# Kernel tuning notes

Measured on AMD Instinct MI355X. Metric: run time of the kernel, lower is better.

## Reference

```python
import jax, jax.numpy as jnp
import numpy as np

H, NH, HD = 1024, 16, 64
B, T, S = 2, 1024, 3
NOISE, STEP, TEMP, NSTEPS = 0.1, 0.01, 1.0, 5
LN_EPS = 1e-5


def setup_inputs() -> dict:
    key = jax.random.key(0)
    ks = jax.random.split(key, 9)
    return {
        "queries": jax.random.normal(ks[0], (B, NH, T, HD), jnp.float32),
        "keys": jax.random.normal(ks[1], (B, NH, T, HD), jnp.float32),
        "values": jax.random.normal(ks[2], (B, NH, T, HD), jnp.float32),
        "hidden_states": jax.random.normal(ks[3], (B, T, H), jnp.float32),
        "W1": jax.random.normal(ks[4], (H, H), jnp.float32) * 0.02,
        "b1": jnp.zeros((H,), jnp.float32),
        "ln_g": jnp.ones((H,), jnp.float32),
        "ln_b": jnp.zeros((H,), jnp.float32),
        "W2": jax.random.normal(ks[5], (H, H), jnp.float32) * 0.02,
        "b2": jnp.zeros((H,), jnp.float32),
        "hyp_noise": jax.random.normal(ks[6], (S, B, NH, T, HD), jnp.float32),
        "ref_noise": jax.random.normal(ks[7], (S, NSTEPS - 1, B, NH, T, HD), jnp.float32),
    }


def _attention_energy(q, k, v):
    # q: [S,B,H,T,D]; k,v: [B,H,T,D] -> energy [S,B]
    scores = jnp.einsum('sbhtd,bhud->sbhtu', q, k) / jnp.sqrt(jnp.float32(q.shape[-1]))
    attn = jax.nn.softmax(scores, axis=-1)
    out = jnp.einsum('sbhtu,bhud->sbhtd', attn, v)
    out_mag = jnp.linalg.norm(out, axis=-1).mean(axis=(2, 3))          # [S,B]
    entropy = -(attn * jnp.log(attn + 1e-8)).sum(axis=-1).mean(axis=(2, 3))
    align = (q * k[None]).sum(axis=-1).mean(axis=(2, 3))
    return out_mag - 0.1 * entropy - 0.05 * align


def reference(queries, keys, values, hidden_states, W1, b1, ln_g, ln_b, W2, b2,
              hyp_noise, ref_noise):
    # query_predictor: Linear -> LayerNorm -> ReLU -> Linear
    x = hidden_states @ W1.T + b1
    mu = x.mean(axis=-1, keepdims=True)
    var = ((x - mu) ** 2).mean(axis=-1, keepdims=True)
    x = (x - mu) / jnp.sqrt(var + LN_EPS) * ln_g + ln_b
    x = jax.nn.relu(x)
    ctx = x @ W2.T + b2                                   # [B,T,H]
    ctx = ctx.reshape(B, T, NH, HD).transpose(0, 2, 1, 3) # [B,NH,T,HD]

    # exploration hypotheses, refined jointly over the sample axis
    q = queries[None] + hyp_noise * NOISE                 # [S,B,NH,T,HD]
    for step in range(NSTEPS):
        q = q - STEP * (q - ctx[None])                    # PCN prediction-error update
        if step < NSTEPS - 1:
            q = q + ref_noise[:, step] * 0.01

    energies = _attention_energy(q, keys, values)         # [S,B]
    probs = jax.nn.softmax(-energies / TEMP, axis=0)      # [S,B]
    selected = jnp.einsum('sb,sbhtd->bhtd', probs, q)     # softmax-weighted mix
    return selected, keys, values
```

## Files before the change

kernel.cpp:

```cpp
#include <hip/hip_runtime.h>
#include <hip/hip_bf16.h>
#include <math.h>

#define NB 2
#define NHH 16
#define TT 1024
#define HDD 64
#define NSS 3
#define HH 1024
#define MMR 2048

typedef float f4 __attribute__((ext_vector_type(4)));
typedef short bf16x8 __attribute__((ext_vector_type(8)));
typedef unsigned short u16;
typedef u16 u16x4 __attribute__((ext_vector_type(4)));

__device__ inline u16 f2bf(float f) {
    union { float f; unsigned u; } v; v.f = f;
    unsigned r = (v.u + 0x7FFFu + ((v.u >> 16) & 1u)) >> 16;
    return (u16)r;
}
__device__ inline float bf2f(u16 u) {
    union { unsigned u; float f; } v; v.u = ((unsigned)u) << 16;
    return v.f;
}

__device__ inline float red16sum(float v) {
    v += __shfl_xor(v, 1);
    v += __shfl_xor(v, 2);
    v += __shfl_xor(v, 4);
    v += __shfl_xor(v, 8);
    return v;
}
__device__ inline float red64sum(float v) {
    v += __shfl_xor(v, 1);
    v += __shfl_xor(v, 2);
    v += __shfl_xor(v, 4);
    v += __shfl_xor(v, 8);
    v += __shfl_xor(v, 16);
    v += __shfl_xor(v, 32);
    return v;
}

__global__ __launch_bounds__(256) void k_cvt4(const float* __restrict__ s0, u16* __restrict__ d0,
                                              const float* __restrict__ s1, u16* __restrict__ d1,
                                              const float* __restrict__ s2, u16* __restrict__ d2,
                                              const float* __restrict__ s3, u16* __restrict__ d3,
                                              float* __restrict__ outk) {
    int b = blockIdx.x;
    if (b >= 4096) {
        int i = (b - 4096) * 256 + threadIdx.x;
        f4 v = ((const f4*)s3)[i];
        ((f4*)outk)[i] = v;
        u16x4 o;
        o[0] = f2bf(v[0] * 0.125f); o[1] = f2bf(v[1] * 0.125f);
        o[2] = f2bf(v[2] * 0.125f); o[3] = f2bf(v[3] * 0.125f);
        ((u16x4*)d3)[i] = o;
        return;
    }
    const float* s; u16* d; int base;
    if (b < 2048)      { s = s0; d = d0; base = 0; }
    else if (b < 3072) { s = s1; d = d1; base = 2048; }
    else               { s = s2; d = d2; base = 3072; }
    int i = (b - base) * 256 + threadIdx.x;
    f4 v = ((const f4*)s)[i];
    u16x4 o;
    o[0] = f2bf(v[0]); o[1] = f2bf(v[1]); o[2] = f2bf(v[2]); o[3] = f2bf(v[3]);
    ((u16x4*)d)[i] = o;
}

__global__ __launch_bounds__(256) void k_vtrans(const float* __restrict__ V,
                                                u16* __restrict__ Vt,
                                                float* __restrict__ outv) {
    __shared__ float tile[64][65];
    int bh = blockIdx.y, t0 = blockIdx.x * 64;
    int r = threadIdx.x >> 2, c0 = (threadIdx.x & 3) * 16;
    const float* vp = V + ((size_t)bh * TT + t0) * HDD;
#pragma unroll
    for (int j = 0; j < 16; j += 4) {
        f4 v = *(const f4*)(vp + r * HDD + c0 + j);
        tile[r][c0 + j + 0] = v[0]; tile[r][c0 + j + 1] = v[1];
        tile[r][c0 + j + 2] = v[2]; tile[r][c0 + j + 3] = v[3];
        *(f4*)(outv + ((size_t)bh * TT + t0 + r) * HDD + c0 + j) = v;
    }
    __syncthreads();
    int d = threadIdx.x >> 2, x0 = (threadIdx.x & 3) * 16;
    u16* op = Vt + ((size_t)bh * HDD + d) * TT + t0 + x0;
#pragma unroll
    for (int j = 0; j < 16; j += 4) {
        u16x4 o;
        o[0] = f2bf(tile[x0 + j + 0][d]); o[1] = f2bf(tile[x0 + j + 1][d]);
        o[2] = f2bf(tile[x0 + j + 2][d]); o[3] = f2bf(tile[x0 + j + 3][d]);
        *(u16x4*)(op + j) = o;
    }
}

template <int EPI>
__global__ __launch_bounds__(256) void k_gemm_bt(const u16* __restrict__ A,
                                                 const u16* __restrict__ Bm,
                                                 const float* __restrict__ bias,
                                                 const float* __restrict__ que,
                                                 float* __restrict__ out) {
    const int K = 1024, N = 1024;
    int w = threadIdx.x >> 6, l = threadIdx.x & 63, lr = l & 15, lg = l >> 4;
    int m0 = blockIdx.y * 64 + w * 16;
    int n0 = blockIdx.x * 64;
    const u16* ap = A + (size_t)(m0 + lr) * K + lg * 8;
    const u16* bp = Bm + (size_t)(n0 + lr) * K + lg * 8;
    f4 z4 = {0.f, 0.f, 0.f, 0.f};
    f4 acc[4] = {z4, z4, z4, z4};
#pragma unroll 2
    for (int kk = 0; kk < K; kk += 32) {
        bf16x8 a  = *(const bf16x8*)(ap + kk);
        bf16x8 b0 = *(const bf16x8*)(bp + kk);
        bf16x8 b1 = *(const bf16x8*)(bp + 16 * K + kk);
        bf16x8 b2 = *(const bf16x8*)(bp + 32 * K + kk);
        bf16x8 b3 = *(const bf16x8*)(bp + 48 * K + kk);
        acc[0] = __builtin_amdgcn_mfma_f32_16x16x32_bf16(a, b0, acc[0], 0, 0, 0);
        acc[1] = __builtin_amdgcn_mfma_f32_16x16x32_bf16(a, b1, acc[1], 0, 0, 0);
        acc[2] = __builtin_amdgcn_mfma_f32_16x16x32_bf16(a, b2, acc[2], 0, 0, 0);
        acc[3] = __builtin_amdgcn_mfma_f32_16x16x32_bf16(a, b3, acc[3], 0, 0, 0);
    }
    const float A5 = 0.9509900499f, CC = 1.0f - A5;
#pragma unroll
    for (int cf = 0; cf < 4; ++cf) {
        int col = n0 + cf * 16 + lr;
        float bs = bias[col];
#pragma unroll
        for (int r = 0; r < 4; ++r) {
            int row = m0 + lg * 4 + r;
            float v = acc[cf][r] + bs;
            if (EPI == 0) {
                out[(size_t)row * N + col] = v;
            } else {
                int b = row >> 10, t = row & 1023, nh = col >> 6, hd = col & 63;
                size_t oidx = (((size_t)(b * NHH + nh)) * TT + t) * HDD + hd;
                out[oidx] = A5 * que[oidx] + CC * v;
            }
        }
    }
}

__global__ __launch_bounds__(256) void k_lnrelu(const float* __restrict__ X,
                                                const float* __restrict__ g,
                                                const float* __restrict__ bta,
                                                u16* __restrict__ xr) {
    int row = blockIdx.x;
    f4 v = ((const f4*)(X + (size_t)row * HH))[threadIdx.x];
    float s = v[0] + v[1] + v[2] + v[3];
    float s2 = v[0] * v[0] + v[1] * v[1] + v[2] * v[2] + v[3] * v[3];
    s = red64sum(s);
    s2 = red64sum(s2);
    __shared__ float red[8];
    int w = threadIdx.x >> 6, l = threadIdx.x & 63;
    if (l == 0) { red[w] = s; red[w + 4] = s2; }
    __syncthreads();
    float S1 = red[0] + red[1] + red[2] + red[3];
    float S2 = red[4] + red[5] + red[6] + red[7];
    float mu = S1 * (1.0f / 1024.0f);
    float var = S2 * (1.0f / 1024.0f) - mu * mu;
    float rstd = rsqrtf(var + 1e-5f);
    f4 gv = ((const f4*)g)[threadIdx.x];
    f4 bv = ((const f4*)bta)[threadIdx.x];
    u16x4 o;
#pragma unroll
    for (int j = 0; j < 4; ++j) {
        float y = (v[j] - mu) * rstd * gv[j] + bv[j];
        y = fmaxf(y, 0.f);
        o[j] = f2bf(y);
    }
    ((u16x4*)(xr + (size_t)row * HH))[threadIdx.x] = o;
}

__global__ __launch_bounds__(256, 3) void k_attn(const float* __restrict__ basep_,
                                                 const float* __restrict__ hyp,
                                                 const float* __restrict__ rn,
                                                 const u16* __restrict__ Kb,
                                                 const u16* __restrict__ Vt,
                                                 u16* __restrict__ qq,
                                                 float* __restrict__ part) {
    int bi = blockIdx.x;
    int p_ = bi & 31, j_ = bi >> 5;
    int h = p_ & 15, b = p_ >> 4;
    int s = j_ >> 3, qt2 = j_ & 7;
    int sb = s * 2 + b;
    int bh = b * NHH + h;
    int pi = sb * 128 + h * 8 + qt2;
    int w = threadIdx.x >> 6, l = threadIdx.x & 63, lr = l & 15, lg = l >> 4;
    int t0 = qt2 * 128;
    f4 z4 = {0.f, 0.f, 0.f, 0.f};

    __shared__ u16 Ks[2][4096];
    __shared__ u16 Vs[2][4096];
    __shared__ u16 plds[8][1024];

    const float CH = 0.1f * 0.9509900499f;
    const float C0 = 0.0096059601f, C1 = 0.0097029900f, C2 = 0.0098010000f, C3 = 0.0099f;
    const float* basep = basep_ + ((size_t)bh * TT) * HDD;
    const float* hypp = hyp + ((size_t)(sb * NHH + h) * TT) * HDD;
    const float* rn0p = rn + ((size_t)(((s * 4 + 0) * 2 + b) * NHH + h) * TT) * HDD;
    const float* rn1p = rn + ((size_t)(((s * 4 + 1) * 2 + b) * NHH + h) * TT) * HDD;
    const float* rn2p = rn + ((size_t)(((s * 4 + 2) * 2 + b) * NHH + h) * TT) * HDD;
    const float* rn3p = rn + ((size_t)(((s * 4 + 3) * 2 + b) * NHH + h) * TT) * HDD;
    u16* qqp = qq + ((size_t)(sb * NHH + h) * TT) * HDD;

    const u16* kbase = Kb + (size_t)bh * TT * HDD;
    const u16* vbase = Vt + (size_t)bh * HDD * TT;
    int u0 = threadIdx.x, u1 = threadIdx.x + 256;
    const u16* kg0 = kbase + u0 * 8;
    const u16* kg1 = kbase + u1 * 8;
    const u16* vg0 = vbase + (size_t)(u0 >> 3) * TT + (u0 & 7) * 8;
    const u16* vg1 = vbase + (size_t)(u1 >> 3) * TT + (u1 & 7) * 8;
    int ko0 = (u0 >> 3) * 128 + (((u0 & 7) ^ ((u0 >> 3) & 7)) << 4);
    int ko1 = (u1 >> 3) * 128 + (((u1 & 7) ^ ((u1 >> 3) & 7)) << 4);

    int4 kr0 = *(const int4*)(kg0);
    int4 kr1 = *(const int4*)(kg1);
    int4 vr0 = *(const int4*)(vg0);
    int4 vr1 = *(const int4*)(vg1);

    char* slab = (char*)&plds[0][0];
    {
        int t = threadIdx.x;
#pragma unroll
        for (int m = 0; m < 4; ++m) {
            int j = t + 256 * m;
            size_t off = (size_t)t0 * HDD + (size_t)j * 8;
            f4 a0 = *(const f4*)(basep + off);
            f4 a1 = *(const f4*)(basep + off + 4);
            a0 += CH * __builtin_nontemporal_load((const f4*)(hypp + off));
            a1 += CH * __builtin_nontemporal_load((const f4*)(hypp + off + 4));
            a0 += C0 * __builtin_nontemporal_load((const f4*)(rn0p + off));
            a1 += C0 * __builtin_nontemporal_load((const f4*)(rn0p + off + 4));
            a0 += C1 * __builtin_nontemporal_load((const f4*)(rn1p + off));
            a1 += C1 * __builtin_nontemporal_load((const f4*)(rn1p + off + 4));
            a0 += C2 * __builtin_nontemporal_load((const f4*)(rn2p + off));
            a1 += C2 * __builtin_nontemporal_load((const f4*)(rn2p + off + 4));
            a0 += C3 * __builtin_nontemporal_load((const f4*)(rn3p + off));
            a1 += C3 * __builtin_nontemporal_load((const f4*)(rn3p + off + 4));
            union { u16 u[8]; int4 i4; } o;
#pragma unroll
            for (int k = 0; k < 4; ++k) { o.u[k] = f2bf(a0[k]); o.u[4 + k] = f2bf(a1[k]); }
            int row = j >> 3, slot = j & 7;
            *(int4*)(slab + row * 128 + (((slot ^ (row & 7))) << 4)) = o.i4;
            *(int4*)(qqp + (size_t)t0 * HDD + (size_t)j * 8) = o.i4;
        }
    }
    *(int4*)((char*)Ks[0] + ko0) = kr0;
    *(int4*)((char*)Ks[0] + ko1) = kr1;
    *(int4*)((char*)Vs[0] + ko0) = vr0;
    *(int4*)((char*)Vs[0] + ko1) = vr1;
    __syncthreads();

    bf16x8 aq[2][2];
#pragma unroll
    for (int qr = 0; qr < 2; ++qr) {
        int r_ = w * 32 + qr * 16 + lr;
#pragma unroll
        for (int c = 0; c < 2; ++c)
            aq[qr][c] = *(const bf16x8*)(slab + r_ * 128 + (((c * 4 + lg) ^ (r_ & 7)) << 4));
    }

    f4 acco[2][4] = {{z4, z4, z4, z4}, {z4, z4, z4, z4}};
    float zrow[2][4] = {{0.f, 0.f, 0.f, 0.f}, {0.f, 0.f, 0.f, 0.f}};
    float wrow[2][4] = {{0.f, 0.f, 0.f, 0.f}, {0.f, 0.f, 0.f, 0.f}};
    float al_lane = 0.f;
    int kdiag = qt2 * 2 + (w >> 1);

    for (int kt = 0; kt < 16; ++kt) {
        int cur = kt & 1;
        if (kt < 15) {
            kr0 = *(const int4*)(kg0 + (kt + 1) * 4096);
            kr1 = *(const int4*)(kg1 + (kt + 1) * 4096);
            vr0 = *(const int4*)(vg0 + (kt + 1) * 64);
            vr1 = *(const int4*)(vg1 + (kt + 1) * 64);
        }
        char* KsB = (char*)Ks[cur];
        char* VsB = (char*)Vs[cur];

        f4 sc[2][4];
#pragma unroll
        for (int cf = 0; cf < 4; ++cf) {
            int row = cf * 16 + lr, rs = row & 7;
            bf16x8 bk0 = *(const bf16x8*)(KsB + row * 128 + ((lg ^ rs) << 4));
            bf16x8 bk1 = *(const bf16x8*)(KsB + row * 128 + (((4 + lg) ^ rs) << 4));
            f4 t0a = __builtin_amdgcn_mfma_f32_16x16x32_bf16(aq[0][0], bk0, z4, 0, 0, 0);
            sc[0][cf] = __builtin_amdgcn_mfma_f32_16x16x32_bf16(aq[0][1], bk1, t0a, 0, 0, 0);
            f4 t1a = __builtin_amdgcn_mfma_f32_16x16x32_bf16(aq[1][0], bk0, z4, 0, 0, 0);
            sc[1][cf] = __builtin_amdgcn_mfma_f32_16x16x32_bf16(aq[1][1], bk1, t1a, 0, 0, 0);
        }

        if (kt == kdiag) {
            f4 sd0 = (w & 1) ? sc[0][2] : sc[0][0];
            f4 sd1 = (w & 1) ? sc[1][3] : sc[1][1];
            int rr = lr & 3;
            float e0 = rr == 0 ? sd0[0] : (rr == 1 ? sd0[1] : (rr == 2 ? sd0[2] : sd0[3]));
            float e1 = rr == 0 ? sd1[0] : (rr == 1 ? sd1[1] : (rr == 2 ? sd1[2] : sd1[3]));
            if (lg == (lr >> 2)) al_lane += (e0 + e1) * 8.0f;
        }

#pragma unroll
        for (int qr = 0; qr < 2; ++qr) {
            u16* pl = &plds[w * 2 + qr][0];
#pragma unroll
            for (int cf = 0; cf < 4; ++cf) {
#pragma unroll
                for (int r = 0; r < 4; ++r) {
                    float sv = sc[qr][cf][r];
                    float pe = __expf(sv);
                    zrow[qr][r] += pe;
                    wrow[qr][r] = fmaf(pe, sv, wrow[qr][r]);
                    int prow = lg * 4 + r;
                    pl[(prow * 64 + cf * 16 + lr) ^ ((prow & 7) << 3)] = f2bf(pe);
                }
            }
        }
        bf16x8 pa[2][2];
#pragma unroll
        for (int qr = 0; qr < 2; ++qr) {
            const u16* pl = &plds[w * 2 + qr][0];
            pa[qr][0] = *(const bf16x8*)&pl[(lr * 64 + lg * 8) ^ ((lr & 7) << 3)];
            pa[qr][1] = *(const bf16x8*)&pl[(lr * 64 + 32 + lg * 8) ^ ((lr & 7) << 3)];
        }
#pragma unroll
        for (int cf = 0; cf < 4; ++cf) {
            int row = cf * 16 + lr, rs = row & 7;
            bf16x8 bv0 = *(const bf16x8*)(VsB + row * 128 + ((lg ^ rs) << 4));
            bf16x8 bv1 = *(const bf16x8*)(VsB + row * 128 + (((4 + lg) ^ rs) << 4));
            acco[0][cf] = __builtin_amdgcn_mfma_f32_16x16x32_bf16(pa[0][0], bv0, acco[0][cf], 0, 0, 0);
            acco[0][cf] = __builtin_amdgcn_mfma_f32_16x16x32_bf16(pa[0][1], bv1, acco[0][cf], 0, 0, 0);
            acco[1][cf] = __builtin_amdgcn_mfma_f32_16x16x32_bf16(pa[1][0], bv0, acco[1][cf], 0, 0, 0);
            acco[1][cf] = __builtin_amdgcn_mfma_f32_16x16x32_bf16(pa[1][1], bv1, acco[1][cf], 0, 0, 0);
        }

        if (kt < 15) {
            char* Kn = (char*)Ks[cur ^ 1];
            char* Vn = (char*)Vs[cur ^ 1];
            *(int4*)(Kn + ko0) = kr0;
            *(int4*)(Kn + ko1) = kr1;
            *(int4*)(Vn + ko0) = vr0;
            *(int4*)(Vn + ko1) = vr1;
        }
        __syncthreads();
    }

    float magw = 0.f, entw = 0.f;
#pragma unroll
    for (int qr = 0; qr < 2; ++qr) {
#pragma unroll
        for (int r = 0; r < 4; ++r) {
            float zz = red16sum(zrow[qr][r]);
            float ww = red16sum(wrow[qr][r]);
            float ssq = acco[qr][0][r] * acco[qr][0][r] + acco[qr][1][r] * acco[qr][1][r] +
                        acco[qr][2][r] * acco[qr][2][r] + acco[qr][3][r] * acco[qr][3][r];
            ssq = red16sum(ssq);
            float inv = 1.0f / zz;
            magw += sqrtf(ssq) * inv;
            entw += __logf(zz) - ww * inv;
        }
    }
    magw += __shfl_xor(magw, 16); magw += __shfl_xor(magw, 32);
    entw += __shfl_xor(entw, 16); entw += __shfl_xor(entw, 32);
    float al = red64sum(al_lane);

    __shared__ float red[4][3];
    if (l == 0) { red[w][0] = magw; red[w][1] = entw; red[w][2] = al; }
    __syncthreads();
    if (threadIdx.x == 0) {
        part[pi * 3 + 0] = red[0][0] + red[1][0] + red[2][0] + red[3][0];
        part[pi * 3 + 1] = red[0][1] + red[1][1] + red[2][1] + red[3][1];
        part[pi * 3 + 2] = red[0][2] + red[1][2] + red[2][2] + red[3][2];
    }
}

__global__ void k_finalize(const float* __restrict__ part, float* __restrict__ probs) {
    int w = threadIdx.x >> 6, l = threadIdx.x & 63;
    __shared__ float eng[6];
    if (w < 6) {
        float a0 = 0.f, a1 = 0.f, a2 = 0.f;
        for (int i = l; i < 128; i += 64) {
            const float* pp = part + (size_t)(w * 128 + i) * 3;
            a0 += pp[0]; a1 += pp[1]; a2 += pp[2];
        }
        a0 = red64sum(a0); a1 = red64sum(a1); a2 = red64sum(a2);
        if (l == 0) {
            const float inv = 1.0f / 16384.0f;
            eng[w] = a0 * inv - 0.1f * (a1 * inv) - 0.05f * (a2 * inv);
        }
    }
    __syncthreads();
    if (threadIdx.x < 2) {
        int b = threadIdx.x;
        float e0 = -eng[0 + b], e1 = -eng[2 + b], e2 = -eng[4 + b];
        float mx = fmaxf(e0, fmaxf(e1, e2));
        float x0 = __expf(e0 - mx), x1 = __expf(e1 - mx), x2 = __expf(e2 - mx);
        float inv = 1.0f / (x0 + x1 + x2);
        probs[0 + b] = x0 * inv;
        probs[2 + b] = x1 * inv;
        probs[4 + b] = x2 * inv;
    }
}

__global__ __launch_bounds__(256) void k_select(const u16* __restrict__ qq,
                                                const float* __restrict__ probs,
                                                float* __restrict__ out) {
    const int NQ4 = 524288;
    int i = blockIdx.x * 256 + threadIdx.x;
    int b = i >> 18;
    float p0 = probs[0 + b], p1 = probs[2 + b], p2 = probs[4 + b];
    u16x4 a0 = ((const u16x4*)qq)[i];
    u16x4 a1 = ((const u16x4*)qq)[NQ4 + i];
    u16x4 a2 = ((const u16x4*)qq)[2 * NQ4 + i];
    f4 v;
#pragma unroll
    for (int j = 0; j < 4; ++j)
        v[j] = p0 * bf2f(a0[j]) + p1 * bf2f(a1[j]) + p2 * bf2f(a2[j]);
    ((f4*)out)[i] = v;
}

extern "C" void kernel_launch(void* const* d_in, const int* in_sizes, int n_in,
                              void* d_out, int out_size, void* d_ws, size_t ws_size,
                              hipStream_t stream) {
    const float* queries = (const float*)d_in[0];
    const float* keys    = (const float*)d_in[1];
    const float* values  = (const float*)d_in[2];
    const float* hs      = (const float*)d_in[3];
    const float* W1      = (const float*)d_in[4];
    const float* b1      = (const float*)d_in[5];
    const float* ln_g    = (const float*)d_in[6];
    const float* ln_b    = (const float*)d_in[7];
    const float* W2      = (const float*)d_in[8];
    const float* b2      = (const float*)d_in[9];
    const float* hyp     = (const float*)d_in[10];
    const float* rn      = (const float*)d_in[11];
    float* out = (float*)d_out;
    char* ws = (char*)d_ws;

    const size_t MB = 1024ull * 1024ull;
    u16*   qq16 = (u16*)(ws);
    u16*   hs_b = (u16*)(ws + 0 * MB);
    u16*   w1_b = (u16*)(ws + 4 * MB);
    u16*   w2_b = (u16*)(ws + 6 * MB);
    float* X    = (float*)(ws + 8 * MB);
    u16*   xr   = (u16*)(ws + 16 * MB);
    float* base = (float*)(ws + 24 * MB);
    u16*   k_b  = (u16*)(ws + 32 * MB);
    u16*   vt_b = (u16*)(ws + 36 * MB);
    float* part = (float*)(ws + 40 * MB);
    float* probs= (float*)(ws + 40 * MB + 65536);

    k_cvt4<<<6144, 256, 0, stream>>>(hs, hs_b, W1, w1_b, W2, w2_b, keys, k_b,
                                     out + 2097152);
    k_vtrans<<<dim3(16, 32), 256, 0, stream>>>(values, vt_b, out + 4194304);

    k_gemm_bt<0><<<dim3(16, 32), 256, 0, stream>>>(hs_b, w1_b, b1, nullptr, X);
    k_lnrelu<<<2048, 256, 0, stream>>>(X, ln_g, ln_b, xr);
    k_gemm_bt<1><<<dim3(16, 32), 256, 0, stream>>>(xr, w2_b, b2, queries, base);

    k_attn<<<768, 256, 0, stream>>>(base, hyp, rn, k_b, vt_b, qq16, part);
    k_finalize<<<1, 384, 0, stream>>>(part, probs);
    k_select<<<2048, 256, 0, stream>>>(qq16, probs, out);
}
```

Baseline: 170.2 us.

## Pre-tile K/V into swizzled bf16 blocks and stream them via direct global-to-LDS loads

Merges the conversion and V-transpose kernels into one prep kernel. That kernel writes K and transposed V as pre-swizzled 64x64 bf16 tiles, so the attention kernel can fill shared memory with global_load_lds instead of a register round-trip. It also stores the first GEMM output as bf16 to halve LN traffic, uses the packed v_cvt_pk_bf16_f32 instruction for conversions, and raises wave priority around the MFMA blocks. The bf16 intermediate before LayerNorm adds some precision loss, and the async LDS loads rely on the existing barrier for correctness.

```diff
diff --git a/kernel.cpp b/kernel.cpp
--- a/kernel.cpp
+++ b/kernel.cpp
@@ -8,7 +8,6 @@
 #define HDD 64
 #define NSS 3
 #define HH 1024
-#define MMR 2048
 
 typedef float f4 __attribute__((ext_vector_type(4)));
 typedef short bf16x8 __attribute__((ext_vector_type(8)));
@@ -23,6 +22,16 @@
 __device__ inline float bf2f(u16 u) {
     union { unsigned u; float f; } v; v.u = ((unsigned)u) << 16;
     return v.f;
+}
+__device__ inline unsigned cvtpk(float lo, float hi) {
+    unsigned r;
+    asm("v_cvt_pk_bf16_f32 %0, %1, %2" : "=v"(r) : "v"(lo), "v"(hi));
+    return r;
+}
+__device__ inline void gl_lds16(const u16* g, u16* l) {
+    __builtin_amdgcn_global_load_lds(
+        (const __attribute__((address_space(1))) unsigned int*)g,
+        (__attribute__((address_space(3))) unsigned int*)l, 16, 0, 0);
 }
 
 __device__ inline float red16sum(float v) {
@@ -42,38 +51,46 @@
     return v;
 }
 
-__global__ __launch_bounds__(256) void k_cvt4(const float* __restrict__ s0, u16* __restrict__ d0,
-                                              const float* __restrict__ s1, u16* __restrict__ d1,
-                                              const float* __restrict__ s2, u16* __restrict__ d2,
-                                              const float* __restrict__ s3, u16* __restrict__ d3,
-                                              float* __restrict__ outk) {
+__global__ __launch_bounds__(256) void k_prep(const float* __restrict__ hs, u16* __restrict__ hs_b,
+                                              const float* __restrict__ W1, u16* __restrict__ w1_b,
+                                              const float* __restrict__ W2, u16* __restrict__ w2_b,
+                                              const float* __restrict__ keys, u16* __restrict__ k_b,
+                                              float* __restrict__ outk,
+                                              const float* __restrict__ V, u16* __restrict__ vt_b,
+                                              float* __restrict__ outv) {
+    __shared__ float tile[64][65];
     int b = blockIdx.x;
-    if (b >= 4096) {
-        int i = (b - 4096) * 256 + threadIdx.x;
-        f4 v = ((const f4*)s3)[i];
-        ((f4*)outk)[i] = v;
+    if (b < 4096) {
+        const float* s; u16* d; int base;
+        if (b < 2048)      { s = hs; d = hs_b; base = 0; }
+        else if (b < 3072) { s = W1; d = w1_b; base = 2048; }
+        else               { s = W2; d = w2_b; base = 3072; }
+        int i = (b - base) * 256 + threadIdx.x;
+        f4 v = ((const f4*)s)[i];
         u16x4 o;
-        o[0] = f2bf(v[0] * 0.125f); o[1] = f2bf(v[1] * 0.125f);
-        o[2] = f2bf(v[2] * 0.125f); o[3] = f2bf(v[3] * 0.125f);
-        ((u16x4*)d3)[i] = o;
+        o[0] = f2bf(v[0]); o[1] = f2bf(v[1]); o[2] = f2bf(v[2]); o[3] = f2bf(v[3]);
+        ((u16x4*)d)[i] = o;
         return;
     }
-    const float* s; u16* d; int base;
-    if (b < 2048)      { s = s0; d = d0; base = 0; }
-    else if (b < 3072) { s = s1; d = d1; base = 2048; }
-    else               { s = s2; d = d2; base = 3072; }
-    int i = (b - base) * 256 + threadIdx.x;
-    f4 v = ((const f4*)s)[i];
-    u16x4 o;
-    o[0] = f2bf(v[0]); o[1] = f2bf(v[1]); o[2] = f2bf(v[2]); o[3] = f2bf(v[3]);
-    ((u16x4*)d)[i] = o;
-}
-
-__global__ __launch_bounds__(256) void k_vtrans(const float* __restrict__ V,
-                                                u16* __restrict__ Vt,
-                                                float* __restrict__ outv) {
-    __shared__ float tile[64][65];
-    int bh = blockIdx.y, t0 = blockIdx.x * 64;
+    if (b < 5120) {
+        int c = (b - 4096) * 256 + threadIdx.x;
+        int bh = c >> 13, t = (c >> 3) & 1023, col8 = c & 7;
+        int kt = t >> 6, row = t & 63;
+        const float* sp = keys + (size_t)c * 8;
+        f4 v0 = *(const f4*)(sp);
+        f4 v1 = *(const f4*)(sp + 4);
+        *(f4*)(outk + (size_t)c * 8) = v0;
+        *(f4*)(outk + (size_t)c * 8 + 4) = v1;
+        union { unsigned u[4]; int4 i4; } o;
+        o.u[0] = cvtpk(v0[0] * 0.125f, v0[1] * 0.125f);
+        o.u[1] = cvtpk(v0[2] * 0.125f, v0[3] * 0.125f);
+        o.u[2] = cvtpk(v1[0] * 0.125f, v1[1] * 0.125f);
+        o.u[3] = cvtpk(v1[2] * 0.125f, v1[3] * 0.125f);
+        *(int4*)(k_b + (size_t)(bh * 16 + kt) * 4096 + row * 64 + ((col8 ^ (row & 7)) << 3)) = o.i4;
+        return;
+    }
+    int idx = b - 5120;
+    int bh = idx >> 4, kt = idx & 15, t0 = kt * 64;
     int r = threadIdx.x >> 2, c0 = (threadIdx.x & 3) * 16;
     const float* vp = V + ((size_t)bh * TT + t0) * HDD;
 #pragma unroll
@@ -85,13 +102,15 @@
     }
     __syncthreads();
     int d = threadIdx.x >> 2, x0 = (threadIdx.x & 3) * 16;
-    u16* op = Vt + ((size_t)bh * HDD + d) * TT + t0 + x0;
-#pragma unroll
-    for (int j = 0; j < 16; j += 4) {
-        u16x4 o;
-        o[0] = f2bf(tile[x0 + j + 0][d]); o[1] = f2bf(tile[x0 + j + 1][d]);
-        o[2] = f2bf(tile[x0 + j + 2][d]); o[3] = f2bf(tile[x0 + j + 3][d]);
-        *(u16x4*)(op + j) = o;
+    u16* op = vt_b + (size_t)(bh * 16 + kt) * 4096 + d * 64;
+#pragma unroll
+    for (int cc = 0; cc < 2; ++cc) {
+        int c8 = (x0 >> 3) + cc;
+        union { unsigned u[4]; int4 i4; } o;
+#pragma unroll
+        for (int p = 0; p < 4; ++p)
+            o.u[p] = cvtpk(tile[c8 * 8 + 2 * p][d], tile[c8 * 8 + 2 * p + 1][d]);
+        *(int4*)(op + ((c8 ^ (d & 7)) << 3)) = o.i4;
     }
 }
 
@@ -100,7 +119,7 @@
                                                  const u16* __restrict__ Bm,
                                                  const float* __restrict__ bias,
                                                  const float* __restrict__ que,
-                                                 float* __restrict__ out) {
+                                                 void* __restrict__ outv) {
     const int K = 1024, N = 1024;
     int w = threadIdx.x >> 6, l = threadIdx.x & 63, lr = l & 15, lg = l >> 4;
     int m0 = blockIdx.y * 64 + w * 16;
@@ -131,22 +150,24 @@
             int row = m0 + lg * 4 + r;
             float v = acc[cf][r] + bs;
             if (EPI == 0) {
-                out[(size_t)row * N + col] = v;
+                ((u16*)outv)[(size_t)row * N + col] = f2bf(v);
             } else {
                 int b = row >> 10, t = row & 1023, nh = col >> 6, hd = col & 63;
                 size_t oidx = (((size_t)(b * NHH + nh)) * TT + t) * HDD + hd;
-                out[oidx] = A5 * que[oidx] + CC * v;
+                ((float*)outv)[oidx] = A5 * que[oidx] + CC * v;
             }
         }
     }
 }
 
-__global__ __launch_bounds__(256) void k_lnrelu(const float* __restrict__ X,
+__global__ __launch_bounds__(256) void k_lnrelu(const u16* __restrict__ X,
                                                 const float* __restrict__ g,
                                                 const float* __restrict__ bta,
                                                 u16* __restrict__ xr) {
     int row = blockIdx.x;
-    f4 v = ((const f4*)(X + (size_t)row * HH))[threadIdx.x];
+    u16x4 xv = ((const u16x4*)(X + (size_t)row * HH))[threadIdx.x];
+    f4 v;
+    v[0] = bf2f(xv[0]); v[1] = bf2f(xv[1]); v[2] = bf2f(xv[2]); v[3] = bf2f(xv[3]);
     float s = v[0] + v[1] + v[2] + v[3];
     float s2 = v[0] * v[0] + v[1] * v[1] + v[2] * v[2] + v[3] * v[3];
     s = red64sum(s);
@@ -194,6 +215,16 @@
     __shared__ u16 Vs[2][4096];
     __shared__ u16 plds[8][1024];
 
+    const u16* kT = Kb + (size_t)(bh * 16) * 4096;
+    const u16* vT = Vt + (size_t)(bh * 16) * 4096;
+
+#pragma unroll
+    for (int j = 0; j < 2; ++j) {
+        int co = (w + 4 * j) * 512;
+        gl_lds16(kT + co + l * 8, &Ks[0][co]);
+        gl_lds16(vT + co + l * 8, &Vs[0][co]);
+    }
+
     const float CH = 0.1f * 0.9509900499f;
     const float C0 = 0.0096059601f, C1 = 0.0097029900f, C2 = 0.0098010000f, C3 = 0.0099f;
     const float* basep = basep_ + ((size_t)bh * TT) * HDD;
@@ -203,21 +234,6 @@
     const float* rn2p = rn + ((size_t)(((s * 4 + 2) * 2 + b) * NHH + h) * TT) * HDD;
     const float* rn3p = rn + ((size_t)(((s * 4 + 3) * 2 + b) * NHH + h) * TT) * HDD;
     u16* qqp = qq + ((size_t)(sb * NHH + h) * TT) * HDD;
-
-    const u16* kbase = Kb + (size_t)bh * TT * HDD;
-    const u16* vbase = Vt + (size_t)bh * HDD * TT;
-    int u0 = threadIdx.x, u1 = threadIdx.x + 256;
-    const u16* kg0 = kbase + u0 * 8;
-    const u16* kg1 = kbase + u1 * 8;
-    const u16* vg0 = vbase + (size_t)(u0 >> 3) * TT + (u0 & 7) * 8;
-    const u16* vg1 = vbase + (size_t)(u1 >> 3) * TT + (u1 & 7) * 8;
-    int ko0 = (u0 >> 3) * 128 + (((u0 & 7) ^ ((u0 >> 3) & 7)) << 4);
-    int ko1 = (u1 >> 3) * 128 + (((u1 & 7) ^ ((u1 >> 3) & 7)) << 4);
-
-    int4 kr0 = *(const int4*)(kg0);
-    int4 kr1 = *(const int4*)(kg1);
-    int4 vr0 = *(const int4*)(vg0);
-    int4 vr1 = *(const int4*)(vg1);
 
     char* slab = (char*)&plds[0][0];
     {
@@ -238,18 +254,14 @@
             a1 += C2 * __builtin_nontemporal_load((const f4*)(rn2p + off + 4));
             a0 += C3 * __builtin_nontemporal_load((const f4*)(rn3p + off));
             a1 += C3 * __builtin_nontemporal_load((const f4*)(rn3p + off + 4));
-            union { u16 u[8]; int4 i4; } o;
-#pragma unroll
-            for (int k = 0; k < 4; ++k) { o.u[k] = f2bf(a0[k]); o.u[4 + k] = f2bf(a1[k]); }
+            union { unsigned u[4]; int4 i4; } o;
+            o.u[0] = cvtpk(a0[0], a0[1]); o.u[1] = cvtpk(a0[2], a0[3]);
+            o.u[2] = cvtpk(a1[0], a1[1]); o.u[3] = cvtpk(a1[2], a1[3]);
             int row = j >> 3, slot = j & 7;
             *(int4*)(slab + row * 128 + (((slot ^ (row & 7))) << 4)) = o.i4;
             *(int4*)(qqp + (size_t)t0 * HDD + (size_t)j * 8) = o.i4;
         }
     }
-    *(int4*)((char*)Ks[0] + ko0) = kr0;
-    *(int4*)((char*)Ks[0] + ko1) = kr1;
-    *(int4*)((char*)Vs[0] + ko0) = vr0;
-    *(int4*)((char*)Vs[0] + ko1) = vr1;
     __syncthreads();
 
     bf16x8 aq[2][2];
@@ -270,15 +282,18 @@
     for (int kt = 0; kt < 16; ++kt) {
         int cur = kt & 1;
         if (kt < 15) {
-            kr0 = *(const int4*)(kg0 + (kt + 1) * 4096);
-            kr1 = *(const int4*)(kg1 + (kt + 1) * 4096);
-            vr0 = *(const int4*)(vg0 + (kt + 1) * 64);
-            vr1 = *(const int4*)(vg1 + (kt + 1) * 64);
+#pragma unroll
+            for (int j = 0; j < 2; ++j) {
+                int co = (w + 4 * j) * 512;
+                gl_lds16(kT + (kt + 1) * 4096 + co + l * 8, &Ks[cur ^ 1][co]);
+                gl_lds16(vT + (kt + 1) * 4096 + co + l * 8, &Vs[cur ^ 1][co]);
+            }
         }
         char* KsB = (char*)Ks[cur];
         char* VsB = (char*)Vs[cur];
 
         f4 sc[2][4];
+        __builtin_amdgcn_s_setprio(1);
 #pragma unroll
         for (int cf = 0; cf < 4; ++cf) {
             int row = cf * 16 + lr, rs = row & 7;
@@ -289,6 +304,7 @@
             f4 t1a = __builtin_amdgcn_mfma_f32_16x16x32_bf16(aq[1][0], bk0, z4, 0, 0, 0);
             sc[1][cf] = __builtin_amdgcn_mfma_f32_16x16x32_bf16(aq[1][1], bk1, t1a, 0, 0, 0);
         }
+        __builtin_amdgcn_s_setprio(0);
 
         if (kt == kdiag) {
             f4 sd0 = (w & 1) ? sc[0][2] : sc[0][0];
@@ -304,15 +320,22 @@
             u16* pl = &plds[w * 2 + qr][0];
 #pragma unroll
             for (int cf = 0; cf < 4; ++cf) {
-#pragma unroll
-                for (int r = 0; r < 4; ++r) {
-                    float sv = sc[qr][cf][r];
-                    float pe = __expf(sv);
-                    zrow[qr][r] += pe;
-                    wrow[qr][r] = fmaf(pe, sv, wrow[qr][r]);
-                    int prow = lg * 4 + r;
-                    pl[(prow * 64 + cf * 16 + lr) ^ ((prow & 7) << 3)] = f2bf(pe);
-                }
+                float p0 = __expf(sc[qr][cf][0]);
+                float p1 = __expf(sc[qr][cf][1]);
+                float p2 = __expf(sc[qr][cf][2]);
+                float p3 = __expf(sc[qr][cf][3]);
+                zrow[qr][0] += p0; zrow[qr][1] += p1;
+                zrow[qr][2] += p2; zrow[qr][3] += p3;
+                wrow[qr][0] = fmaf(p0, sc[qr][cf][0], wrow[qr][0]);
+                wrow[qr][1] = fmaf(p1, sc[qr][cf][1], wrow[qr][1]);
+                wrow[qr][2] = fmaf(p2, sc[qr][cf][2], wrow[qr][2]);
+                wrow[qr][3] = fmaf(p3, sc[qr][cf][3], wrow[qr][3]);
+                unsigned pa01 = cvtpk(p0, p1), pa23 = cvtpk(p2, p3);
+                int base_ = cf * 16 + lr;
+                pl[(((lg * 4 + 0) * 64 + base_)) ^ (((lg * 4 + 0) & 7) << 3)] = (u16)pa01;
+                pl[(((lg * 4 + 1) * 64 + base_)) ^ (((lg * 4 + 1) & 7) << 3)] = (u16)(pa01 >> 16);
+                pl[(((lg * 4 + 2) * 64 + base_)) ^ (((lg * 4 + 2) & 7) << 3)] = (u16)pa23;
+                pl[(((lg * 4 + 3) * 64 + base_)) ^ (((lg * 4 + 3) & 7) << 3)] = (u16)(pa23 >> 16);
             }
         }
         bf16x8 pa[2][2];
@@ -322,6 +345,7 @@
             pa[qr][0] = *(const bf16x8*)&pl[(lr * 64 + lg * 8) ^ ((lr & 7) << 3)];
             pa[qr][1] = *(const bf16x8*)&pl[(lr * 64 + 32 + lg * 8) ^ ((lr & 7) << 3)];
         }
+        __builtin_amdgcn_s_setprio(1);
 #pragma unroll
         for (int cf = 0; cf < 4; ++cf) {
             int row = cf * 16 + lr, rs = row & 7;
@@ -332,15 +356,8 @@
             acco[1][cf] = __builtin_amdgcn_mfma_f32_16x16x32_bf16(pa[1][0], bv0, acco[1][cf], 0, 0, 0);
             acco[1][cf] = __builtin_amdgcn_mfma_f32_16x16x32_bf16(pa[1][1], bv1, acco[1][cf], 0, 0, 0);
         }
-
-        if (kt < 15) {
-            char* Kn = (char*)Ks[cur ^ 1];
-            char* Vn = (char*)Vs[cur ^ 1];
-            *(int4*)(Kn + ko0) = kr0;
-            *(int4*)(Kn + ko1) = kr1;
-            *(int4*)(Vn + ko0) = vr0;
-            *(int4*)(Vn + ko1) = vr1;
-        }
+        __builtin_amdgcn_s_setprio(0);
+
         __syncthreads();
     }
 
@@ -441,7 +458,7 @@
     u16*   hs_b = (u16*)(ws + 0 * MB);
     u16*   w1_b = (u16*)(ws + 4 * MB);
     u16*   w2_b = (u16*)(ws + 6 * MB);
-    float* X    = (float*)(ws + 8 * MB);
+    u16*   X    = (u16*)(ws + 8 * MB);
     u16*   xr   = (u16*)(ws + 16 * MB);
     float* base = (float*)(ws + 24 * MB);
     u16*   k_b  = (u16*)(ws + 32 * MB);
@@ -449,9 +466,9 @@
     float* part = (float*)(ws + 40 * MB);
     float* probs= (float*)(ws + 40 * MB + 65536);
 
-    k_cvt4<<<6144, 256, 0, stream>>>(hs, hs_b, W1, w1_b, W2, w2_b, keys, k_b,
-                                     out + 2097152);
-    k_vtrans<<<dim3(16, 32), 256, 0, stream>>>(values, vt_b, out + 4194304);
+    k_prep<<<5632, 256, 0, stream>>>(hs, hs_b, W1, w1_b, W2, w2_b,
+                                     keys, k_b, out + 2097152,
+                                     values, vt_b, out + 4194304);
 
     k_gemm_bt<0><<<dim3(16, 32), 256, 0, stream>>>(hs_b, w1_b, b1, nullptr, X);
     k_lnrelu<<<2048, 256, 0, stream>>>(X, ln_g, ln_b, xr);
```

Result: no change. 167.4 us (-1.7%).
